# Performance work log

Measured on AMD Instinct MI355X. Metric: run time of the kernel, lower is better.

## Reference

```python
import jax, jax.numpy as jnp
import numpy as np
from jax import lax

PRE_NMS = 2000
POST_NMS = 300
NMS_THRESH = 0.7
MIN_SIZE = 16.0
SCALE = 1.0
RATIOS = (0.5, 1.0, 2.0)
SCALES = (8, 16, 32)
STRIDES = (8, 16, 32)
FEAT_HW = ((100, 100), (50, 50), (25, 25))
BASE_SIZE = 16.0


def _anchor_base(scale):
    py = px = BASE_SIZE / 2.0
    ab = np.zeros((len(RATIOS), 4), dtype=np.float32)
    for i, r in enumerate(RATIOS):
        h = BASE_SIZE * scale * np.sqrt(r)
        w = BASE_SIZE * scale * np.sqrt(1.0 / r)
        ab[i] = [py - h / 2.0, px - w / 2.0, py + h / 2.0, px + w / 2.0]
    return ab


def _enum_anchors():
    out = []
    for lvl in range(3):
        ab = _anchor_base(SCALES[lvl])
        hh, ww = FEAT_HW[lvl]
        fs = STRIDES[lvl]
        sy = np.arange(0, hh * fs, fs)
        sx = np.arange(0, ww * fs, fs)
        sx, sy = np.meshgrid(sx, sy)
        shift = np.stack((sy.ravel(), sx.ravel(), sy.ravel(), sx.ravel()), axis=1)
        a = ab[None, :, :] + shift[:, None, :]  # [K, A, 4]
        out.append(a.reshape(-1, 4).astype(np.float32))
    return np.concatenate(out, axis=0)  # [39375, 4]


def setup_inputs() -> dict:
    key = jax.random.key(0)
    ks = jax.random.split(key, 8)
    inp = {
        "feat0": jax.random.normal(ks[0], (2, 256, 100, 100), jnp.float32),
        "feat1": jax.random.normal(ks[1], (2, 256, 50, 50), jnp.float32),
        "feat2": jax.random.normal(ks[2], (2, 256, 25, 25), jnp.float32),
        "conv_w": 0.01 * jax.random.normal(ks[3], (256, 256, 3, 3), jnp.float32),
        "conv_b": jnp.zeros((256,), jnp.float32),
        "score_w": 0.01 * jax.random.normal(ks[4], (6, 256), jnp.float32),
        "score_b": jnp.zeros((6,), jnp.float32),
        "loc_w": 0.01 * jax.random.normal(ks[5], (12, 256), jnp.float32),
        "loc_b": jnp.zeros((12,), jnp.float32),
        "anchors": jnp.asarray(_enum_anchors()),
        "img_h": 800,
        "img_w": 800,
    }
    return inp


def loc2bbox(anchors, loc):
    src_h = anchors[:, 2] - anchors[:, 0]
    src_w = anchors[:, 3] - anchors[:, 1]
    ctr_y = anchors[:, 0] + 0.5 * src_h
    ctr_x = anchors[:, 1] + 0.5 * src_w
    dy, dx, dh, dw = loc[:, 0], loc[:, 1], loc[:, 2], loc[:, 3]
    cy = dy * src_h + ctr_y
    cx = dx * src_w + ctr_x
    h = jnp.exp(dh) * src_h
    w = jnp.exp(dw) * src_w
    return jnp.stack([cy - 0.5 * h, cx - 0.5 * w, cy + 0.5 * h, cx + 0.5 * w], axis=1)


def _iou_matrix(boxes):
    area = (boxes[:, 2] - boxes[:, 0]) * (boxes[:, 3] - boxes[:, 1])
    tl = jnp.maximum(boxes[:, None, :2], boxes[None, :, :2])
    br = jnp.minimum(boxes[:, None, 2:], boxes[None, :, 2:])
    wh = jnp.clip(br - tl, 0.0)
    inter = wh[..., 0] * wh[..., 1]
    return inter / (area[:, None] + area[None, :] - inter + 1e-12)


def _nms_keep(boxes, valid):
    # greedy NMS over score-sorted boxes; returns boolean keep mask
    M = _iou_matrix(boxes)  # [PRE_NMS, PRE_NMS]
    idx = jnp.arange(PRE_NMS)

    def body(i, suppressed):
        sup_later = (~suppressed[i]) & (M[i] > NMS_THRESH) & (idx > i)
        return suppressed | sup_later

    suppressed = lax.fori_loop(0, PRE_NMS, body, ~valid)
    return ~suppressed


def _propose(loc, fg, anchors, img_h, img_w):
    roi = loc2bbox(anchors, loc)  # [S, 4]
    roi = jnp.stack([
        jnp.clip(roi[:, 0], 0.0, float(img_h)),
        jnp.clip(roi[:, 1], 0.0, float(img_w)),
        jnp.clip(roi[:, 2], 0.0, float(img_h)),
        jnp.clip(roi[:, 3], 0.0, float(img_w)),
    ], axis=1)
    hs = roi[:, 2] - roi[:, 0]
    ws = roi[:, 3] - roi[:, 1]
    valid = (hs >= MIN_SIZE * SCALE) & (ws >= MIN_SIZE * SCALE)
    sc = jnp.where(valid, fg, -jnp.inf)
    top_sc, top_idx = lax.top_k(sc, PRE_NMS)
    boxes = roi[top_idx]
    keep = _nms_keep(boxes, jnp.isfinite(top_sc))
    # stable move of kept boxes to the front (indices are unique)
    order = jnp.argsort(jnp.where(keep, jnp.arange(PRE_NMS), PRE_NMS))[:POST_NMS]
    rois = boxes[order] * keep[order][:, None].astype(boxes.dtype)  # zero-pad invalid
    return rois  # [POST_NMS, 4]


def reference(feat0, feat1, feat2, conv_w, conv_b, score_w, score_b, loc_w, loc_b, anchors, img_h, img_w):
    feats = [feat0, feat1, feat2]
    n = feat0.shape[0]
    locs, scores, fgs = [], [], []
    dn = ("NCHW", "OIHW", "NCHW")
    for x in feats:
        h = jax.nn.relu(
            lax.conv_general_dilated(x, conv_w, (1, 1), "SAME", dimension_numbers=dn)
            + conv_b[None, :, None, None]
        )
        hh, ww = h.shape[2], h.shape[3]
        loc = jnp.einsum("nchw,oc->nhwo", h, loc_w) + loc_b  # [n,h,w,12]
        sc = jnp.einsum("nchw,oc->nhwo", h, score_w) + score_b  # [n,h,w,6]
        fg = jax.nn.softmax(sc.reshape(n, hh, ww, 3, 2), axis=-1)[..., 1]
        locs.append(loc.reshape(n, -1, 4))
        scores.append(sc.reshape(n, -1, 2))
        fgs.append(fg.reshape(n, -1))
    rpn_locs = jnp.concatenate(locs, axis=1)      # [n, S, 4]
    rpn_scores = jnp.concatenate(scores, axis=1)  # [n, S, 2]
    rpn_fg = jnp.concatenate(fgs, axis=1)         # [n, S]
    rois = jax.vmap(lambda l, f: _propose(l, f, anchors, img_h, img_w))(rpn_locs, rpn_fg)
    rois = rois.reshape(-1, 4)  # [n*POST_NMS, 4]
    roi_indices = jnp.repeat(jnp.arange(n, dtype=jnp.int32), POST_NMS)
    return rpn_locs, rpn_scores, rois, roi_indices, anchors
```

## Files before the change

kernel.cpp:

```cpp
#include <hip/hip_runtime.h>
#include <hip/hip_fp16.h>
#include <cstdint>
#include <cstddef>

typedef unsigned long long u64;
typedef unsigned int u32;
typedef __attribute__((ext_vector_type(8))) _Float16 f16x8;
typedef __attribute__((ext_vector_type(4))) float f32x4;

#define NANCHORS 39375
#define PRE_NMS  2000
#define POST_NMS 300
#define CAND_CAP 4096
#define MPAD 2048
#define UNEG 0x007FFFFFu

__device__ __forceinline__ u32 f2u(float f) {
  u32 u = __float_as_uint(f);
  return (u & 0x80000000u) ? ~u : (u | 0x80000000u);
}

#define GLOAD16(gp, lp) __builtin_amdgcn_global_load_lds( \
    (const __attribute__((address_space(1))) u32*)(const void*)(gp), \
    (__attribute__((address_space(3))) u32*)(void*)(lp), 16, 0, 0)

__global__ __launch_bounds__(256) void xsplit_kernel(
    const float* __restrict__ f0, const float* __restrict__ f1, const float* __restrict__ f2,
    short* __restrict__ xh, short* __restrict__ xl)
{
  __shared__ float tile[64][65];
  int t = blockIdx.x;
  int HW, W, W2, np; const float* fp; int AB, ABS;
  if (t < 1256)      { HW = 10000; W = 100; W2 = 102; np = 157; fp = f0; AB = 0;       ABS = 2663424; }
  else if (t < 1576) { t -= 1256; HW = 2500; W = 50; W2 = 52; np = 40; fp = f1; AB = 5326848; ABS = 692224; }
  else               { t -= 1576; HW = 625;  W = 25; W2 = 27; np = 10; fp = f2; AB = 6711296; ABS = 186624; }
  int posb = t % np, r = t / np;
  int ci0 = (r & 3) * 64, b = r >> 2;
  int pos0 = posb * 64;
  int tid = threadIdx.x, lane = tid & 63, w = tid >> 6;
  int rp = pos0 + lane; if (rp >= HW) rp = HW - 1;
  const float* src = fp + (size_t)(b * 256 + ci0) * HW;
#pragma unroll
  for (int p = 0; p < 16; ++p) {
    int cl = w * 16 + p;
    tile[cl][lane] = src[(size_t)cl * HW + rp];
  }
  __syncthreads();
  int pix = tid >> 2, cq = tid & 3;
  int pos = pos0 + pix;
  if (pos < HW) {
    int y = pos / W, x = pos - y * W;
    size_t ob = (size_t)AB + (size_t)b * ABS + ((size_t)((y + 1) * W2 + (x + 1))) * 256 + ci0 + cq * 16;
    __align__(16) short hs[16], ls[16];
#pragma unroll
    for (int j = 0; j < 16; ++j) {
      float v = tile[cq * 16 + j][pix];
      __half h = __float2half(v);
      __half l = __float2half((v - __half2float(h)) * 2048.0f);
      hs[j] = __half_as_short(h);
      ls[j] = __half_as_short(l);
    }
    *(int4*)(xh + ob) = ((int4*)hs)[0];
    *(int4*)(xh + ob + 8) = ((int4*)hs)[1];
    *(int4*)(xl + ob) = ((int4*)ls)[0];
    *(int4*)(xl + ob + 8) = ((int4*)ls)[1];
  }
}

__global__ __launch_bounds__(256) void wsplit_kernel(
    const float* __restrict__ w, short* __restrict__ wh, short* __restrict__ wl)
{
  int idx = blockIdx.x * 256 + threadIdx.x;
  int tap = idx >> 16, co = (idx >> 8) & 255, ci = idx & 255;
  float v = w[(size_t)co * 2304 + ci * 9 + tap];
  __half h = __float2half(v);
  __half l = __float2half((v - __half2float(h)) * 2048.0f);
  wh[idx] = __half_as_short(h);
  wl[idx] = __half_as_short(l);
}

__global__ __launch_bounds__(256, 2) void gemmconv_kernel(
    const short* __restrict__ xh, const short* __restrict__ xl,
    const short* __restrict__ wh, const short* __restrict__ wl,
    const float* __restrict__ bias, float* __restrict__ hbase)
{
  __shared__ __align__(16) short smem[32768];

  int lb = (blockIdx.x & 7) * 52 + (blockIdx.x >> 3);
  int HW, W, W2, AB, ABS; size_t hoff;
  if (lb < 316)      { HW = 10000; W = 100; W2 = 102; AB = 0;       ABS = 2663424; hoff = 0; }
  else if (lb < 396) { lb -= 316; HW = 2500; W = 50; W2 = 52; AB = 5326848; ABS = 692224; hoff = 5120000; }
  else               { lb -= 396; HW = 625;  W = 25; W2 = 27; AB = 6711296; ABS = 186624; hoff = 6400000; }
  int mb = lb >> 2, b = (lb >> 1) & 1, nb = lb & 1;
  int pos0 = mb * 128, co0 = nb * 128;

  int tid = threadIdx.x;
  int s = tid & 7, mrow = tid >> 3;
  int aoff[4], boff[4];
#pragma unroll
  for (int i = 0; i < 4; ++i) {
    int m = i * 32 + mrow;
    int pos = pos0 + m; if (pos >= HW) pos = HW - 1;
    int y = pos / W, x = pos - y * W;
    aoff[i] = AB + b * ABS + (y * W2 + x) * 256 + ((s ^ (m & 7)) << 3);
    boff[i] = ((co0 + m) << 8) + ((s ^ (m & 7)) << 3);
  }
  int wv = tid >> 6, lane = tid & 63;
  int lr = lane & 15, lk = lane >> 4;
  int wr = wv >> 1, wc = wv & 1;
  int rA0 = wr * 64 + lr, rB0 = wc * 64 + lr;
  int cs = (lr & 7) << 4;
  int c0 = ((lk * 16) ^ cs) >> 1;
  int c1 = ((64 + lk * 16) ^ cs) >> 1;

  f32x4 acc1[4][4], acc2[4][4];
  f32x4 zro = {0.f, 0.f, 0.f, 0.f};
#pragma unroll
  for (int i = 0; i < 4; ++i)
#pragma unroll
    for (int j = 0; j < 4; ++j) { acc1[i][j] = zro; acc2[i][j] = zro; }

  for (int cc = 0; cc < 36; ++cc) {
    int tap = cc >> 2, cq = cc & 3;
    int ty = tap / 3, tx = tap - ty * 3;
    int adel = (ty * W2 + tx) * 256 + (cq << 6);
    int bdel = (tap << 16) + (cq << 6);
    if (cc) __syncthreads();
#pragma unroll
    for (int i = 0; i < 4; ++i) {
      int d = i * 2048 + wv * 512;
      GLOAD16(xh + aoff[i] + adel, smem + d);
      GLOAD16(xl + aoff[i] + adel, smem + 8192 + d);
      GLOAD16(wh + boff[i] + bdel, smem + 16384 + d);
      GLOAD16(wl + boff[i] + bdel, smem + 24576 + d);
    }
    __syncthreads();
#pragma unroll
    for (int k2 = 0; k2 < 2; ++k2) {
      int ck = k2 ? c1 : c0;
      f16x8 ah[4], al[4], bh[4], bl[4];
#pragma unroll
      for (int q = 0; q < 4; ++q) {
        int ro = (rA0 + q * 16) * 64 + ck;
        ah[q] = *(const f16x8*)(smem + ro);
        al[q] = *(const f16x8*)(smem + 8192 + ro);
        int rb = (rB0 + q * 16) * 64 + ck;
        bh[q] = *(const f16x8*)(smem + 16384 + rb);
        bl[q] = *(const f16x8*)(smem + 24576 + rb);
      }
#pragma unroll
      for (int m4 = 0; m4 < 4; ++m4)
#pragma unroll
        for (int n4 = 0; n4 < 4; ++n4) {
          acc1[m4][n4] = __builtin_amdgcn_mfma_f32_16x16x32_f16(ah[m4], bh[n4], acc1[m4][n4], 0, 0, 0);
          acc2[m4][n4] = __builtin_amdgcn_mfma_f32_16x16x32_f16(ah[m4], bl[n4], acc2[m4][n4], 0, 0, 0);
          acc2[m4][n4] = __builtin_amdgcn_mfma_f32_16x16x32_f16(al[m4], bh[n4], acc2[m4][n4], 0, 0, 0);
        }
    }
  }

  float br[4];
#pragma unroll
  for (int n4 = 0; n4 < 4; ++n4) br[n4] = bias[co0 + wc * 64 + n4 * 16 + lr];
  float* outb = hbase + hoff + (size_t)b * HW * 256;
#pragma unroll
  for (int m4 = 0; m4 < 4; ++m4) {
#pragma unroll
    for (int j = 0; j < 4; ++j) {
      int pos = pos0 + wr * 64 + m4 * 16 + lk * 4 + j;
      if (pos < HW) {
        float* op = outb + (size_t)pos * 256 + co0 + wc * 64 + lr;
#pragma unroll
        for (int n4 = 0; n4 < 4; ++n4)
          op[n4 * 16] = acc1[m4][n4][j] + acc2[m4][n4][j] * 4.8828125e-4f + br[n4];
      }
    }
  }
}

__global__ __launch_bounds__(256) void head_kernel(
    const float* __restrict__ hbase, const float* __restrict__ loc_w, const float* __restrict__ loc_b,
    const float* __restrict__ score_w, const float* __restrict__ score_b,
    const float* __restrict__ anchors, const int* __restrict__ imgh, const int* __restrict__ imgw,
    float* __restrict__ out_locs, float* __restrict__ out_scores,
    float* __restrict__ boxes, u32* __restrict__ ukey)
{
  __shared__ float wT[4 * 1288];
  int tid = threadIdx.x;
  for (int idx = tid; idx < 4608; idx += 256) {
    int o = idx >> 8, c = idx & 255;
    float v = (o < 12) ? loc_w[o * 256 + c] : score_w[(o - 12) * 256 + c];
    wT[(c >> 6) * 1288 + (c & 63) * 20 + o] = v;
  }
  for (int idx = tid; idx < 512; idx += 256) {
    int c = idx >> 1, o = 18 + (idx & 1);
    wT[(c >> 6) * 1288 + (c & 63) * 20 + o] = 0.f;
  }
  __syncthreads();

  int t = blockIdx.x;
  int b = t / 207, r = t % 207;
  int HW, pos0, base_row; size_t hoff;
  if (r < 157)      { HW = 10000; pos0 = r * 64;         base_row = 0;     hoff = 0; }
  else if (r < 197) { HW = 2500;  pos0 = (r - 157) * 64; base_row = 30000; hoff = 5120000; }
  else              { HW = 625;   pos0 = (r - 197) * 64; base_row = 37500; hoff = 6400000; }

  int px = tid >> 2, q = tid & 3;
  int pos = pos0 + px;
  int pc = (pos < HW) ? pos : HW - 1;
  const float* hp = hbase + hoff + ((size_t)b * HW + pc) * 256 + q * 64;
  const float* wq = wT + q * 1288;

  f32x4 acc[5];
#pragma unroll
  for (int o4 = 0; o4 < 5; ++o4) acc[o4] = (f32x4){0.f, 0.f, 0.f, 0.f};

#pragma unroll 4
  for (int i = 0; i < 16; ++i) {
    float4 hv = *(const float4*)(hp + i * 4);
    float hk[4] = {fmaxf(hv.x, 0.f), fmaxf(hv.y, 0.f), fmaxf(hv.z, 0.f), fmaxf(hv.w, 0.f)};
#pragma unroll
    for (int k = 0; k < 4; ++k) {
      const float4* wrow = (const float4*)(wq + (i * 4 + k) * 20);
#pragma unroll
      for (int o4 = 0; o4 < 5; ++o4) {
        float4 wv = wrow[o4];
        acc[o4][0] = fmaf(hk[k], wv.x, acc[o4][0]);
        acc[o4][1] = fmaf(hk[k], wv.y, acc[o4][1]);
        acc[o4][2] = fmaf(hk[k], wv.z, acc[o4][2]);
        acc[o4][3] = fmaf(hk[k], wv.w, acc[o4][3]);
      }
    }
  }
#pragma unroll
  for (int o4 = 0; o4 < 5; ++o4)
#pragma unroll
    for (int cpo = 0; cpo < 4; ++cpo) {
      float v = acc[o4][cpo];
      v += __shfl_xor(v, 1, 64);
      v += __shfl_xor(v, 2, 64);
      acc[o4][cpo] = v;
    }

  if (q == 0 && pos < HW) {
    float sarr[18] = {acc[0][0], acc[0][1], acc[0][2], acc[0][3],
                      acc[1][0], acc[1][1], acc[1][2], acc[1][3],
                      acc[2][0], acc[2][1], acc[2][2], acc[2][3],
                      acc[3][0], acc[3][1], acc[3][2], acc[3][3],
                      acc[4][0], acc[4][1]};
    float IH = (float)(*imgh), IW = (float)(*imgw);
#pragma unroll
    for (int a = 0; a < 3; ++a) {
      float l0 = sarr[4 * a + 0] + loc_b[4 * a + 0];
      float l1 = sarr[4 * a + 1] + loc_b[4 * a + 1];
      float l2 = sarr[4 * a + 2] + loc_b[4 * a + 2];
      float l3 = sarr[4 * a + 3] + loc_b[4 * a + 3];
      float sc0 = sarr[12 + 2 * a + 0] + score_b[2 * a + 0];
      float sc1 = sarr[12 + 2 * a + 1] + score_b[2 * a + 1];

      int row = base_row + pos * 3 + a;
      size_t g = (size_t)b * NANCHORS + row;
      *(float4*)(out_locs + g * 4) = make_float4(l0, l1, l2, l3);
      out_scores[g * 2 + 0] = sc0; out_scores[g * 2 + 1] = sc1;

      float mx = fmaxf(sc0, sc1);
      float e0 = expf(sc0 - mx), e1 = expf(sc1 - mx);
      float fg = e1 / (e0 + e1);

      const float* an = anchors + (size_t)row * 4;
      float a0 = an[0], a1 = an[1], a2 = an[2], a3 = an[3];
      float sh = a2 - a0, sw = a3 - a1;
      float cy = a0 + 0.5f * sh, cx = a1 + 0.5f * sw;
      float ncy = l0 * sh + cy, ncx = l1 * sw + cx;
      float nh = expf(l2) * sh, nw = expf(l3) * sw;
      float y1 = fminf(fmaxf(ncy - 0.5f * nh, 0.f), IH);
      float x1 = fminf(fmaxf(ncx - 0.5f * nw, 0.f), IW);
      float y2 = fminf(fmaxf(ncy + 0.5f * nh, 0.f), IH);
      float x2 = fminf(fmaxf(ncx + 0.5f * nw, 0.f), IW);
      bool valid = ((y2 - y1) >= 16.0f) && ((x2 - x1) >= 16.0f);
      float scm = valid ? fg : -__builtin_inff();

      *(float4*)(boxes + g * 4) = make_float4(y1, x1, y2, x2);
      ukey[g] = f2u(scm);
    }
  }
}

__global__ void copyf_kernel(const float* __restrict__ a, float* __restrict__ o, int n) {
  int t = blockIdx.x * 256 + threadIdx.x;
  if (t < n) o[t] = a[t];
}

__global__ __launch_bounds__(1024) void selectsort_kernel(
    const u32* __restrict__ ukey, const float* __restrict__ boxes,
    float* __restrict__ topbox, u64* __restrict__ sup0)
{
  int b = blockIdx.x, tid = threadIdx.x;
  int wv = tid >> 6;
  const u32* u = ukey + (size_t)b * NANCHORS;
  __shared__ u32 hist[16][256];
  __shared__ u32 scan[256];
  __shared__ u32 sh_prefix;
  __shared__ int sh_rem;
  __shared__ int sh_cnt;
  __shared__ u64 key[CAND_CAP];
  __shared__ unsigned char validf[2048];

  u32 prefix = 0; int rem = PRE_NMS;
  for (int pass = 0; pass < 4; ++pass) {
    int shift = 24 - 8 * pass;
    for (int i = tid; i < 16 * 256; i += 1024) ((u32*)hist)[i] = 0;
    __syncthreads();
    u32 himask = (pass == 0) ? 0u : (0xFFFFFFFFu << (shift + 8));
    for (int i = tid; i < NANCHORS; i += 1024) {
      u32 v = u[i];
      if ((v & himask) == (prefix & himask))
        atomicAdd(&hist[wv][(v >> shift) & 255u], 1u);
    }
    __syncthreads();
    if (tid < 256) {
      u32 s = 0;
#pragma unroll
      for (int k = 0; k < 16; ++k) s += hist[k][tid];
      scan[tid] = s;
    }
    __syncthreads();
    for (int off = 1; off < 256; off <<= 1) {
      u32 v = 0, add = 0;
      if (tid < 256) { v = scan[tid]; if (tid + off < 256) add = scan[tid + off]; }
      __syncthreads();
      if (tid < 256) scan[tid] = v + add;
      __syncthreads();
    }
    if (tid < 256) {
      int s = (int)scan[tid];
      int snext = (tid < 255) ? (int)scan[tid + 1] : 0;
      if (s >= rem && snext < rem) { sh_prefix = prefix | ((u32)tid << shift); sh_rem = rem - snext; }
    }
    __syncthreads();
    prefix = sh_prefix; rem = sh_rem;
    __syncthreads();
  }

  if (tid == 0) sh_cnt = 0;
  __syncthreads();
  for (int i = tid; i < NANCHORS; i += 1024) {
    u32 v = u[i];
    if (v >= prefix) {
      int p = atomicAdd(&sh_cnt, 1);
      if (p < CAND_CAP)
        key[p] = ((u64)v << 32) | (u32)(~(u32)i);
    }
  }
  __syncthreads();
  int cnt = (sh_cnt < CAND_CAP) ? sh_cnt : CAND_CAP;
  for (int t = tid; t < CAND_CAP; t += 1024)
    if (t >= cnt) key[t] = 0ull;
  __syncthreads();

  u32 n = (cnt <= 2048) ? 2048u : (u32)CAND_CAP;
  for (u32 k = 2; k <= n; k <<= 1) {
    for (u32 j = k >> 1; j > 0; j >>= 1) {
      __syncthreads();
      for (u32 t = tid; t < n; t += 1024) {
        u32 ixj = t ^ j;
        if (ixj > t) {
          u64 a = key[t], c = key[ixj];
          bool desc = ((t & k) == 0);
          if (desc ? (a < c) : (a > c)) { key[t] = c; key[ixj] = a; }
        }
      }
    }
  }
  __syncthreads();

  for (int t = tid; t < 2048; t += 1024) {
    unsigned char vf = 0;
    if (t < PRE_NMS) {
      u64 kk = key[t];
      u32 uu = (u32)(kk >> 32);
      float* tb = topbox + ((size_t)b * PRE_NMS + t) * 4;
      if (uu != 0u) {
        u32 idx = ~((u32)kk);
        const float* bp = boxes + ((size_t)b * NANCHORS + idx) * 4;
        tb[0] = bp[0]; tb[1] = bp[1]; tb[2] = bp[2]; tb[3] = bp[3];
        vf = (uu != UNEG) ? 1 : 0;
      } else {
        tb[0] = 0.f; tb[1] = 0.f; tb[2] = 0.f; tb[3] = 0.f;
      }
    }
    validf[t] = vf;
  }
  __syncthreads();
  if (tid < 32) {
    u64 m = 0;
    for (int bit = 0; bit < 64; ++bit) {
      int j = tid * 64 + bit;
      if (j >= PRE_NMS || !validf[j]) m |= (1ull << bit);
    }
    sup0[b * 32 + tid] = m;
  }
}

__global__ __launch_bounds__(256) void iou_kernel(const float* __restrict__ topbox, u32* __restrict__ M32)
{
  int t = blockIdx.x * 256 + threadIdx.x;
  int b = blockIdx.y;
  int w = t / 2000, i = t % 2000;
  const float* tb = topbox + (size_t)b * PRE_NMS * 4;
  const float* bi = tb + (size_t)i * 4;
  float iy1 = bi[0], ix1 = bi[1], iy2 = bi[2], ix2 = bi[3];
  float ai = (iy2 - iy1) * (ix2 - ix1);
  u64 m = 0;
  for (int bit = 0; bit < 64; ++bit) {
    int j = w * 64 + bit;
    if (j < PRE_NMS && j > i) {
      const float* bj = tb + (size_t)j * 4;
      float ty = fmaxf(iy1, bj[0]), tx = fmaxf(ix1, bj[1]);
      float by = fminf(iy2, bj[2]), bx = fminf(ix2, bj[3]);
      float hh = fmaxf(by - ty, 0.f), ww = fmaxf(bx - tx, 0.f);
      float inter = hh * ww;
      float aj = (bj[2] - bj[0]) * (bj[3] - bj[1]);
      float iou = inter / (ai + aj - inter + 1e-12f);
      if (iou > 0.7f) m |= (1ull << bit);
    }
  }
  u32* out = M32 + (size_t)b * MPAD * 64;
  out[(size_t)(2 * w)     * MPAD + i] = (u32)m;
  out[(size_t)(2 * w + 1) * MPAD + i] = (u32)(m >> 32);
}

__global__ __launch_bounds__(320) void final_kernel(
    const u32* __restrict__ M32, const u64* __restrict__ sup0, const float* __restrict__ topbox,
    float* __restrict__ rois, float* __restrict__ roiidx)
{
  int b = blockIdx.x, tid = threadIdx.x;
  __shared__ u32 supl[64];
  __shared__ int ord[POST_NMS];
  __shared__ int cnt_s;

  if (tid < 64) {
    int l = tid;
    const u32* col = M32 + (size_t)b * MPAD * 64 + (size_t)l * MPAD;
    u32 sup = ((const u32*)sup0)[b * 64 + l];
    uint4 A[16], B[16];
#pragma unroll
    for (int k = 0; k < 16; ++k) A[k] = *(const uint4*)(col + 4 * k);

#define NMS_PROC(buf, cc) do {                                                     \
  _Pragma("unroll")                                                                \
  for (int rr = 0; rr < 64; ++rr) {                                                \
    u32 d = ((rr & 3) == 0) ? buf[rr >> 2].x : ((rr & 3) == 1) ? buf[rr >> 2].y :  \
            ((rr & 3) == 2) ? buf[rr >> 2].z : buf[rr >> 2].w;                     \
    u32 sb = (u32)__builtin_amdgcn_readlane((int)sup, 2 * (cc) + (rr >> 5));       \
    u32 m = ((sb >> (rr & 31)) & 1u) - 1u;                                         \
    sup |= m & d;                                                                  \
  } } while (0)

    for (int c = 0; c < 32; c += 2) {
#pragma unroll
      for (int k = 0; k < 16; ++k) B[k] = *(const uint4*)(col + (c + 1) * 64 + 4 * k);
      NMS_PROC(A, c);
      if (c + 2 < 32) {
#pragma unroll
        for (int k = 0; k < 16; ++k) A[k] = *(const uint4*)(col + (c + 2) * 64 + 4 * k);
      }
      NMS_PROC(B, c + 1);
    }
    supl[l] = sup;
  }
  __syncthreads();
  if (tid == 0) {
    int cnt = 0;
    for (int w = 0; w < 64 && cnt < POST_NMS; ++w) {
      u32 kept = ~supl[w];
      while (kept && cnt < POST_NMS) {
        int bit = __builtin_ctz(kept); kept &= kept - 1;
        ord[cnt++] = w * 32 + bit;
      }
    }
    cnt_s = cnt;
  }
  __syncthreads();
  if (tid < POST_NMS) {
    float v0 = 0.f, v1 = 0.f, v2 = 0.f, v3 = 0.f;
    if (tid < cnt_s) {
      const float* tb = topbox + ((size_t)b * PRE_NMS + ord[tid]) * 4;
      v0 = tb[0]; v1 = tb[1]; v2 = tb[2]; v3 = tb[3];
    }
    float* r = rois + ((size_t)b * POST_NMS + tid) * 4;
    r[0] = v0; r[1] = v1; r[2] = v2; r[3] = v3;
    roiidx[b * POST_NMS + tid] = (float)b;
  }
}

extern "C" void kernel_launch(void* const* d_in, const int* in_sizes, int n_in,
                              void* d_out, int out_size, void* d_ws, size_t ws_size,
                              hipStream_t stream) {
  const float* feat0   = (const float*)d_in[0];
  const float* feat1   = (const float*)d_in[1];
  const float* feat2   = (const float*)d_in[2];
  const float* conv_w  = (const float*)d_in[3];
  const float* conv_b  = (const float*)d_in[4];
  const float* score_w = (const float*)d_in[5];
  const float* score_b = (const float*)d_in[6];
  const float* loc_w   = (const float*)d_in[7];
  const float* loc_b   = (const float*)d_in[8];
  const float* anchors = (const float*)d_in[9];
  const int*   img_h   = (const int*)d_in[10];
  const int*   img_w   = (const int*)d_in[11];

  float* out_f       = (float*)d_out;
  float* out_locs    = out_f;
  float* out_scores  = out_f + 315000;
  float* out_rois    = out_f + 472500;
  float* out_roiidx  = out_f + 474900;
  float* out_anchors = out_f + 475500;

  char* p = (char*)d_ws;
  float* hb = (float*)p;      p += (size_t)6720000 * 4;
  short* xth = (short*)p;     p += (size_t)7084544 * 2;
  short* xtl = (short*)p;     p += (size_t)7084544 * 2;
  short* wsh = (short*)p;     p += (size_t)589824 * 2;
  short* wsl = (short*)p;     p += (size_t)589824 * 2;
  float* boxes = (float*)p;   p += (size_t)315000 * 4;
  u32* ukey = (u32*)p;        p += (size_t)78752 * 4;
  float* topbox = (float*)p;  p += (size_t)16000 * 4;
  u32* M32 = (u32*)p;         p += (size_t)2 * MPAD * 64 * 4;
  u64* sup0 = (u64*)p;        p += 64 * 8;

  hipMemsetAsync(xth, 0, (size_t)7084544 * 4, stream);
  xsplit_kernel<<<1656, 256, 0, stream>>>(feat0, feat1, feat2, xth, xtl);
  wsplit_kernel<<<2304, 256, 0, stream>>>(conv_w, wsh, wsl);
  gemmconv_kernel<<<416, 256, 0, stream>>>(xth, xtl, wsh, wsl, conv_b, hb);
  head_kernel<<<414, 256, 0, stream>>>(
      hb, loc_w, loc_b, score_w, score_b, anchors, img_h, img_w,
      out_locs, out_scores, boxes, ukey);
  copyf_kernel<<<(157500 + 255) / 256, 256, 0, stream>>>(anchors, out_anchors, 157500);
  selectsort_kernel<<<2, 1024, 0, stream>>>(ukey, boxes, topbox, sup0);
  iou_kernel<<<dim3(250, 2), 256, 0, stream>>>(topbox, M32);
  final_kernel<<<2, 320, 0, stream>>>(M32, sup0, topbox, out_rois, out_roiidx);
}
```

Measured before the change: 370.7 us.

## Cache keys in registers and use wave-aggregated atomics in radix select

The selectsort kernel now loads each thread's 39 keys into registers once instead of re-reading global memory on each of four radix passes and the compaction pass. Histogram updates aggregate lanes that share the leader's bin into one atomic, and a single 256-bin histogram replaces per-wave histograms. The prefix scan becomes a 64-lane shuffle scan, and compaction uses one ballot-based atomic per wave. This trades higher register pressure and possible atomic contention on a single histogram for fewer global reads and fewer barriers.

```diff
diff --git a/kernel.cpp b/kernel.cpp
--- a/kernel.cpp
+++ b/kernel.cpp
@@ -296,60 +296,91 @@
     float* __restrict__ topbox, u64* __restrict__ sup0)
 {
   int b = blockIdx.x, tid = threadIdx.x;
-  int wv = tid >> 6;
+  int lane = tid & 63;
   const u32* u = ukey + (size_t)b * NANCHORS;
-  __shared__ u32 hist[16][256];
-  __shared__ u32 scan[256];
+  __shared__ u32 hist[256];
   __shared__ u32 sh_prefix;
   __shared__ int sh_rem;
   __shared__ int sh_cnt;
   __shared__ u64 key[CAND_CAP];
   __shared__ unsigned char validf[2048];
 
+  u32 val[39];
+#pragma unroll
+  for (int k = 0; k < 38; ++k) val[k] = u[tid + k * 1024];
+  val[38] = (tid < 463) ? u[tid + 38912] : 0u;
+
   u32 prefix = 0; int rem = PRE_NMS;
+#pragma unroll 1
   for (int pass = 0; pass < 4; ++pass) {
     int shift = 24 - 8 * pass;
-    for (int i = tid; i < 16 * 256; i += 1024) ((u32*)hist)[i] = 0;
+    if (tid < 256) hist[tid] = 0;
     __syncthreads();
     u32 himask = (pass == 0) ? 0u : (0xFFFFFFFFu << (shift + 8));
-    for (int i = tid; i < NANCHORS; i += 1024) {
-      u32 v = u[i];
-      if ((v & himask) == (prefix & himask))
-        atomicAdd(&hist[wv][(v >> shift) & 255u], 1u);
+    u32 pmask = prefix & himask;
+#pragma unroll
+    for (int k = 0; k < 39; ++k) {
+      bool live = (k < 38) || (tid < 463);
+      u32 v = val[k];
+      bool m = live && ((v & himask) == pmask);
+      u32 bin = (v >> shift) & 255u;
+      u64 actm = __ballot(m);
+      if (actm) {
+        int src = __ffsll(actm) - 1;
+        u32 binf = __shfl(bin, src, 64);
+        bool same = m && (bin == binf);
+        u64 sm = __ballot(same);
+        if (same) {
+          if (lane == __ffsll(sm) - 1)
+            atomicAdd(&hist[binf], (u32)__popcll(sm));
+        } else if (m) {
+          atomicAdd(&hist[bin], 1u);
+        }
+      }
     }
     __syncthreads();
-    if (tid < 256) {
-      u32 s = 0;
-#pragma unroll
-      for (int k = 0; k < 16; ++k) s += hist[k][tid];
-      scan[tid] = s;
-    }
-    __syncthreads();
-    for (int off = 1; off < 256; off <<= 1) {
-      u32 v = 0, add = 0;
-      if (tid < 256) { v = scan[tid]; if (tid + off < 256) add = scan[tid + off]; }
-      __syncthreads();
-      if (tid < 256) scan[tid] = v + add;
-      __syncthreads();
-    }
-    if (tid < 256) {
-      int s = (int)scan[tid];
-      int snext = (tid < 255) ? (int)scan[tid + 1] : 0;
-      if (s >= rem && snext < rem) { sh_prefix = prefix | ((u32)tid << shift); sh_rem = rem - snext; }
+    if (tid < 64) {
+      u32 h0 = hist[4 * lane], h1 = hist[4 * lane + 1];
+      u32 h2 = hist[4 * lane + 2], h3 = hist[4 * lane + 3];
+      u32 L = h0 + h1 + h2 + h3;
+      u32 SS = L;
+#pragma unroll
+      for (int off = 1; off < 64; off <<= 1) {
+        u32 tv = __shfl_down(SS, off, 64);
+        if (lane + off < 64) SS += tv;
+      }
+      u32 T = SS - L;
+      u32 s3 = h3 + T, s2 = h2 + s3, s1 = h1 + s2, s0 = h0 + s1;
+      u32 sv[5] = {s0, s1, s2, s3, T};
+#pragma unroll
+      for (int j = 0; j < 4; ++j) {
+        if ((int)sv[j] >= rem && (int)sv[j + 1] < rem) {
+          sh_prefix = prefix | ((u32)(4 * lane + j) << shift);
+          sh_rem = rem - (int)sv[j + 1];
+        }
+      }
     }
     __syncthreads();
     prefix = sh_prefix; rem = sh_rem;
-    __syncthreads();
   }
 
   if (tid == 0) sh_cnt = 0;
   __syncthreads();
-  for (int i = tid; i < NANCHORS; i += 1024) {
-    u32 v = u[i];
-    if (v >= prefix) {
-      int p = atomicAdd(&sh_cnt, 1);
-      if (p < CAND_CAP)
-        key[p] = ((u64)v << 32) | (u32)(~(u32)i);
+#pragma unroll
+  for (int k = 0; k < 39; ++k) {
+    bool live = (k < 38) || (tid < 463);
+    u32 v = val[k];
+    bool c = live && (v >= prefix);
+    u64 mask = __ballot(c);
+    if (mask) {
+      int leader = __ffsll(mask) - 1;
+      int cntw = __popcll(mask);
+      int base = 0;
+      if (lane == leader) base = atomicAdd(&sh_cnt, cntw);
+      base = __shfl(base, leader, 64);
+      int p = base + (int)__popcll(mask & ((1ull << lane) - 1ull));
+      if (c && p < CAND_CAP)
+        key[p] = ((u64)v << 32) | (u32)(~(u32)(tid + k * 1024));
     }
   }
   __syncthreads();
```

Result: faster. 361.4 us (-2.5%).
